# Performance work log

Hardware: AMD Instinct MI355X
Metric: run time of the kernel (lower is better)

The kernel has to match this reference:

```python
import jax, jax.numpy as jnp
import numpy as np

SIM_THRES = 0.9
CLASS_SPEC = True
CIN, COUT, K, H, W_DIM = 256, 64, 1024, 200, 400


def setup_inputs() -> dict:
    key = jax.random.key(0)
    k1, k2, k3, k4, k5 = jax.random.split(key, 5)
    idx_feat = jax.random.normal(k1, (1, CIN, K, 1), jnp.float32)
    x = jax.random.normal(k2, (1, COUT, H * W_DIM), jnp.float32)
    W = jax.random.normal(k3, (COUT, CIN), jnp.float32) * 0.01  # conv1x1 weight, init std=0.01
    b = jnp.zeros((COUT,), jnp.float32)
    pred_cate = jax.random.randint(k4, (K,), 0, 80)
    pred_score = jax.random.uniform(k5, (K,), jnp.float32)
    return {"x": x, "idx_feat": idx_feat, "pred_cate": pred_cate,
            "pred_score": pred_score, "W": W, "b": b, "n": 1, "h": H, "w": W_DIM}


def reference(x, idx_feat, pred_cate, pred_score, W, b, n, h, w):
    # 1x1 conv -> reshape -> permute: meta_weight [K, Cout]
    feat = idx_feat[0, :, :, 0]                      # [Cin, K]
    mw = feat.T @ W.T + b                            # [K, Cout]
    # cosine similarity (row-normalized, clamp min 1e-8)
    nrm = jnp.linalg.norm(mw, axis=1, keepdims=True)
    a = mw / jnp.maximum(nrm, 1e-8)
    sim = a @ a.T                                    # [K, K]
    label = jnp.triu(sim >= SIM_THRES)
    if CLASS_SPEC:
        label = label & (pred_cate[:, None] == pred_cate[None, :])
    # cumsum-based greedy Matrix-NMS-style dedup
    cum = jnp.cumsum(label.astype(jnp.float32), axis=0) < 2.0
    keep = jnp.diagonal(cum)                         # [K] bool keep mask
    # masked rows instead of boolean indexing (jit-static shapes);
    # non-kept rows are zeroed and their norm replaced by 1 to avoid 0/0.
    lm = (label & cum).astype(jnp.float32) * keep[:, None].astype(jnp.float32)
    ln = lm.sum(axis=1, keepdims=True)
    merged = (lm @ mw) / jnp.where(ln > 0, ln, 1.0)  # [K, Cout]
    inst = jnp.einsum('kc,ncp->nkp', merged, x).reshape(n, -1, h, w)
    return inst, keep, pred_cate, pred_score
```

## Files before the change

kernel.cpp:

```cpp
#include <hip/hip_runtime.h>
#include <math.h>

#define CIN 256
#define COUT 64
#define KN 1024
#define PN 80000
#define SIMT 0.9f

typedef __attribute__((ext_vector_type(8))) short  short8;
typedef __attribute__((ext_vector_type(4))) float  f32x4;

__device__ inline unsigned short f2bf(float f) {
    unsigned u = __float_as_uint(f);
    unsigned r = u + 0x7FFFu + ((u >> 16) & 1u);
    return (unsigned short)(r >> 16);
}

__global__ __launch_bounds__(256) void k_mw(const float* __restrict__ idx_feat,
                                            const float* __restrict__ W,
                                            const float* __restrict__ b,
                                            float* __restrict__ mw,
                                            float* __restrict__ a) {
    int t = threadIdx.x;
    int id = blockIdx.x * 256 + t;
    int k = id >> 6;
    int o = id & 63;
    const float4* W4 = (const float4*)W;
    float acc = 0.f;
    #pragma unroll 4
    for (int c4 = 0; c4 < 64; ++c4) {
        float4 wv = W4[o * 64 + c4];
        int c = c4 * 4;
        acc += idx_feat[(c + 0) * KN + k] * wv.x
             + idx_feat[(c + 1) * KN + k] * wv.y
             + idx_feat[(c + 2) * KN + k] * wv.z
             + idx_feat[(c + 3) * KN + k] * wv.w;
    }
    float v = acc + b[o];
    mw[k * COUT + o] = v;
    float ss = v * v;
    #pragma unroll
    for (int m = 1; m < 64; m <<= 1) ss += __shfl_xor(ss, m, 64);
    float nrm = sqrtf(ss);
    a[k * COUT + o] = v / fmaxf(nrm, 1e-8f);
}

__global__ __launch_bounds__(256) void k_label(const float* __restrict__ a,
                                               const int* __restrict__ cate,
                                               unsigned int* __restrict__ mask,
                                               unsigned int* __restrict__ keep) {
    int j = blockIdx.x;
    int t = threadIdx.x;
    __shared__ __align__(16) float ajs[64];
    __shared__ int cnts[256];
    __shared__ unsigned int mws[32];
    if (t < 64) ajs[t] = a[j * 64 + t];
    if (t < 32) mws[t] = 0u;
    __syncthreads();
    int cj = cate[j];
    const float4* a4  = (const float4*)a;
    const float4* aj4 = (const float4*)ajs;
    bool lab[4];
    int cnt = 0;
    #pragma unroll
    for (int q = 0; q < 4; ++q) {
        int i = t * 4 + q;
        float s = 0.f;
        #pragma unroll
        for (int c4 = 0; c4 < 16; ++c4) {
            float4 av = a4[i * 16 + c4];
            float4 jv = aj4[c4];
            s += av.x * jv.x + av.y * jv.y + av.z * jv.z + av.w * jv.w;
        }
        lab[q] = (i <= j) && (s >= SIMT) && (cate[i] == cj);
        cnt += lab[q] ? 1 : 0;
    }
    cnts[t] = cnt;
    __syncthreads();
    for (int off = 1; off < 256; off <<= 1) {
        int v = cnts[t];
        int add = (t >= off) ? cnts[t - off] : 0;
        __syncthreads();
        cnts[t] = v + add;
        __syncthreads();
    }
    int run = cnts[t] - cnt;
    #pragma unroll
    for (int q = 0; q < 4; ++q) {
        int i = t * 4 + q;
        run += lab[q] ? 1 : 0;
        bool cumf = run < 2;
        if (lab[q] && cumf) atomicOr(&mws[i >> 5], 1u << (i & 31));
        if (i == j) keep[j] = cumf ? 1u : 0u;
    }
    __syncthreads();
    if (t < 32) mask[j * 32 + t] = mws[t];
}

__global__ __launch_bounds__(256) void k_merge(const float* __restrict__ mw,
                                               const unsigned int* __restrict__ mask,
                                               const unsigned int* __restrict__ keep,
                                               unsigned short* __restrict__ mergedB) {
    int i = blockIdx.x;
    int t = threadIdx.x;
    int c = t & 63, g = t >> 6;
    int wi = i >> 5;
    unsigned int bi = 1u << (i & 31);
    float acc = 0.f;
    int cnt = 0;
    for (int jj = 0; jj < 256; ++jj) {
        int j = g * 256 + jj;
        unsigned int wv = mask[j * 32 + wi];
        if (wv & bi) { acc += mw[j * 64 + c]; cnt++; }
    }
    __shared__ float sa[4][64];
    __shared__ int sc[4];
    sa[g][c] = acc;
    if (c == 0) sc[g] = cnt;
    __syncthreads();
    if (g == 0) {
        float tot = sa[0][c] + sa[1][c] + sa[2][c] + sa[3][c];
        int ct = sc[0] + sc[1] + sc[2] + sc[3];
        float mv = keep[i] ? tot / (float)max(ct, 1) : 0.f;
        mergedB[i * 64 + c] = f2bf(mv);
    }
}

__global__ __launch_bounds__(256) void k_inst(const float* __restrict__ x,
                                              const unsigned short* __restrict__ mergedB,
                                              float* __restrict__ out) {
    int t = threadIdx.x;
    int lane = t & 63;
    int wv = t >> 6;
    int n0 = blockIdx.x * 64 + wv * 16;
    int m0 = blockIdx.y * 512;
    int nn = n0 + (lane & 15);
    int quad = lane >> 4;

    short8 bfr[2];
    #pragma unroll
    for (int f = 0; f < 2; ++f) {
        #pragma unroll
        for (int j = 0; j < 8; ++j) {
            int k = f * 32 + quad * 8 + j;
            bfr[f][j] = (short)f2bf(x[k * PN + nn]);
        }
    }

    int arow_off = quad * 8;
    #pragma unroll 4
    for (int mt = 0; mt < 32; ++mt) {
        int mrow = m0 + mt * 16 + (lane & 15);
        const unsigned short* ap = mergedB + mrow * 64 + arow_off;
        short8 a0 = *(const short8*)(ap);
        short8 a1 = *(const short8*)(ap + 32);
        f32x4 acc = {0.f, 0.f, 0.f, 0.f};
        acc = __builtin_amdgcn_mfma_f32_16x16x32_bf16(a0, bfr[0], acc, 0, 0, 0);
        acc = __builtin_amdgcn_mfma_f32_16x16x32_bf16(a1, bfr[1], acc, 0, 0, 0);
        int rbase = m0 + mt * 16 + quad * 4;
        #pragma unroll
        for (int r = 0; r < 4; ++r) {
            out[(rbase + r) * PN + nn] = acc[r];
        }
    }
}

__global__ void k_tail(const int* __restrict__ cate,
                       const float* __restrict__ score,
                       const unsigned int* __restrict__ keep,
                       float* __restrict__ out) {
    int t = blockIdx.x * 256 + threadIdx.x;
    if (t < KN) {
        long base = (long)KN * PN;
        out[base + t]            = keep[t] ? 1.f : 0.f;
        out[base + KN + t]       = (float)cate[t];
        out[base + 2 * KN + t]   = score[t];
    }
}

extern "C" void kernel_launch(void* const* d_in, const int* in_sizes, int n_in,
                              void* d_out, int out_size, void* d_ws, size_t ws_size,
                              hipStream_t stream) {
    const float* x        = (const float*)d_in[0];
    const float* idx_feat = (const float*)d_in[1];
    const int*   cate     = (const int*)d_in[2];
    const float* score    = (const float*)d_in[3];
    const float* W        = (const float*)d_in[4];
    const float* b        = (const float*)d_in[5];
    float* out = (float*)d_out;

    char* ws = (char*)d_ws;
    float*          mw      = (float*)(ws + 0);
    float*          a       = (float*)(ws + 262144);
    unsigned short* mergedB = (unsigned short*)(ws + 524288);
    unsigned int*   mask    = (unsigned int*)(ws + 655360);
    unsigned int*   keep    = (unsigned int*)(ws + 786432);

    k_mw   <<<256,  256, 0, stream>>>(idx_feat, W, b, mw, a);
    k_label<<<KN,   256, 0, stream>>>(a, cate, mask, keep);
    k_merge<<<KN,   256, 0, stream>>>(mw, mask, keep, mergedB);
    dim3 gD(PN / 64, 2);
    k_inst <<<gD,   256, 0, stream>>>(x, mergedB, out);
    k_tail <<<4,    256, 0, stream>>>(cate, score, keep, out);
}
```

Measured before the change: 526.4 us.

## Transpose MFMA operands for vectorized output stores and fold tail into inst kernel

```diff
diff --git a/kernel.cpp b/kernel.cpp
--- a/kernel.cpp
+++ b/kernel.cpp
@@ -128,53 +128,46 @@
 
 __global__ __launch_bounds__(256) void k_inst(const float* __restrict__ x,
                                               const unsigned short* __restrict__ mergedB,
+                                              const int* __restrict__ cate,
+                                              const float* __restrict__ score,
+                                              const unsigned int* __restrict__ keep,
                                               float* __restrict__ out) {
     int t = threadIdx.x;
     int lane = t & 63;
     int wv = t >> 6;
-    int n0 = blockIdx.x * 64 + wv * 16;
-    int m0 = blockIdx.y * 512;
-    int nn = n0 + (lane & 15);
+    int l15 = lane & 15;
     int quad = lane >> 4;
+    int p0 = blockIdx.x * 64 + wv * 16;
+    int pp = p0 + l15;
 
-    short8 bfr[2];
+    short8 a0, a1;
     #pragma unroll
-    for (int f = 0; f < 2; ++f) {
-        #pragma unroll
-        for (int j = 0; j < 8; ++j) {
-            int k = f * 32 + quad * 8 + j;
-            bfr[f][j] = (short)f2bf(x[k * PN + nn]);
-        }
+    for (int j = 0; j < 8; ++j) {
+        int c = quad * 8 + j;
+        a0[j] = (short)f2bf(x[c * PN + pp]);
+        a1[j] = (short)f2bf(x[(c + 32) * PN + pp]);
     }
 
-    int arow_off = quad * 8;
     #pragma unroll 4
-    for (int mt = 0; mt < 32; ++mt) {
-        int mrow = m0 + mt * 16 + (lane & 15);
-        const unsigned short* ap = mergedB + mrow * 64 + arow_off;
-        short8 a0 = *(const short8*)(ap);
-        short8 a1 = *(const short8*)(ap + 32);
+    for (int kt = 0; kt < 64; ++kt) {
+        int k0 = kt * 16;
+        const unsigned short* bp = mergedB + (k0 + l15) * 64 + quad * 8;
+        short8 b0 = *(const short8*)(bp);
+        short8 b1 = *(const short8*)(bp + 32);
         f32x4 acc = {0.f, 0.f, 0.f, 0.f};
-        acc = __builtin_amdgcn_mfma_f32_16x16x32_bf16(a0, bfr[0], acc, 0, 0, 0);
-        acc = __builtin_amdgcn_mfma_f32_16x16x32_bf16(a1, bfr[1], acc, 0, 0, 0);
-        int rbase = m0 + mt * 16 + quad * 4;
-        #pragma unroll
-        for (int r = 0; r < 4; ++r) {
-            out[(rbase + r) * PN + nn] = acc[r];
+        acc = __builtin_amdgcn_mfma_f32_16x16x32_bf16(a0, b0, acc, 0, 0, 0);
+        acc = __builtin_amdgcn_mfma_f32_16x16x32_bf16(a1, b1, acc, 0, 0, 0);
+        float4 v = {acc[0], acc[1], acc[2], acc[3]};
+        *(float4*)(out + (k0 + l15) * PN + p0 + quad * 4) = v;
+    }
+
+    if (blockIdx.x == 0) {
+        long base = (long)KN * PN;
+        for (int i = t; i < KN; i += 256) {
+            out[base + i]            = keep[i] ? 1.f : 0.f;
+            out[base + KN + i]       = (float)cate[i];
+            out[base + 2 * KN + i]   = score[i];
         }
-    }
-}
-
-__global__ void k_tail(const int* __restrict__ cate,
-                       const float* __restrict__ score,
-                       const unsigned int* __restrict__ keep,
-                       float* __restrict__ out) {
-    int t = blockIdx.x * 256 + threadIdx.x;
-    if (t < KN) {
-        long base = (long)KN * PN;
-        out[base + t]            = keep[t] ? 1.f : 0.f;
-        out[base + KN + t]       = (float)cate[t];
-        out[base + 2 * KN + t]   = score[t];
     }
 }
 
@@ -199,7 +192,5 @@
     k_mw   <<<256,  256, 0, stream>>>(idx_feat, W, b, mw, a);
     k_label<<<KN,   256, 0, stream>>>(a, cate, mask, keep);
     k_merge<<<KN,   256, 0, stream>>>(mw, mask, keep, mergedB);
-    dim3 gD(PN / 64, 2);
-    k_inst <<<gD,   256, 0, stream>>>(x, mergedB, out);
-    k_tail <<<4,    256, 0, stream>>>(cate, score, keep, out);
+    k_inst <<<PN / 64, 256, 0, stream>>>(x, mergedB, cate, score, keep, out);
 }
```

Measured after the change: 528.5 us. No clear change (+0.4%).
